# Optimization experiments

Hardware: AMD Instinct MI355X
Metric: run time of the kernel (lower is better)

Reference implementation:

```python
import jax, jax.numpy as jnp
import numpy as np

N = 100000   # nodes
E = 1000000  # edges
G = 2000     # graphs
ND = 64      # node_dim (== hidden_dim so per-layer params stack)
ED = 16      # edge_dim
HD = 64      # hidden_dim
L = 4        # num_layers


def setup_inputs() -> dict:
    key = jax.random.key(0)
    ks = jax.random.split(key, 16)
    s = 0.1  # param init scale
    return {
        "x": jax.random.normal(ks[0], (N, ND), jnp.float32),
        "edge_index": jax.random.randint(ks[1], (2, E), 0, N, jnp.int32),
        "edge_attr": jax.random.normal(ks[2], (E, ED), jnp.float32),
        "batch": jnp.sort(jax.random.randint(ks[3], (N,), 0, G, jnp.int32)),
        "t_cond": jax.random.uniform(ks[4], (G,), jnp.float32),
        # per-layer GINEConv params (stacked over L layers)
        "lin_e": jax.random.normal(ks[5], (L, ED, ND), jnp.float32) * s,  # edge_attr -> in_dim
        "W1": jax.random.normal(ks[6], (L, ND, HD), jnp.float32) * s,
        "b1": jnp.zeros((L, HD), jnp.float32),
        "W2": jax.random.normal(ks[7], (L, HD, HD), jnp.float32) * s,
        "b2": jnp.zeros((L, HD), jnp.float32),
        "eps": jnp.zeros((L,), jnp.float32),  # train_eps=True, init 0
        # head: Linear(HD+1 -> HD), ReLU, Linear(HD -> 1)
        "head_W1": jax.random.normal(ks[8], (HD + 1, HD), jnp.float32) * s,
        "head_b1": jnp.zeros((HD,), jnp.float32),
        "head_W2": jax.random.normal(ks[9], (HD, 1), jnp.float32) * s,
        "head_b2": jnp.zeros((1,), jnp.float32),
    }


def reference(x, edge_index, edge_attr, batch, t_cond,
              lin_e, W1, b1, W2, b2, eps,
              head_W1, head_b1, head_W2, head_b2):
    src = edge_index[0]  # x_j (message source)
    dst = edge_index[1]  # x_i (aggregation target)
    for l in range(L):
        # GINEConv: m_ij = ReLU(x_j + Lin(edge_attr)); aggr = sum_j m_ij
        e = edge_attr @ lin_e[l]                      # [E, ND]
        m = jax.nn.relu(x[src] + e)                   # gather + fuse
        aggr = jax.ops.segment_sum(m, dst, num_segments=N)  # scatter-add [N, ND]
        h = (1.0 + eps[l]) * x + aggr
        x = jax.nn.relu(h @ W1[l] + b1[l]) @ W2[l] + b2[l]  # nn_seq MLP
        x = jax.nn.relu(x)  # outer ReLU (dropout off at inference)
    # global mean pool over graphs
    sums = jax.ops.segment_sum(x, batch, num_segments=G)          # [G, HD]
    cnts = jax.ops.segment_sum(jnp.ones((N, 1), x.dtype), batch, num_segments=G)
    pooled = sums / jnp.maximum(cnts, 1.0)
    h = jnp.concatenate([pooled, t_cond[:, None].astype(x.dtype)], axis=-1)  # [G, HD+1]
    out = jax.nn.relu(h @ head_W1 + head_b1) @ head_W2 + head_b2             # [G, 1]
    return out
```

## Files before the change

kernel.cpp:

```cpp
#include <hip/hip_runtime.h>

#define NDIM 64
#define EDIM 16
#define SCAN_BS 256
#define SCAN_TILE 2048

typedef __attribute__((ext_vector_type(8))) short short8;
typedef __attribute__((ext_vector_type(4))) float f32x4;
typedef __attribute__((ext_vector_type(4))) float f4;

#define AS4 __attribute__((address_space(4)))
__device__ inline const AS4 int* cs_i(const int* p) {
    return (const AS4 int*)(unsigned long long)p;
}
__device__ inline const AS4 f4* cs_f4(const float* p) {
    return (const AS4 f4*)(unsigned long long)p;
}

__device__ inline unsigned short f2bf_rne(float f) {
    unsigned int u = __float_as_uint(f);
    unsigned int r = u + 0x7FFFu + ((u >> 16) & 1u);
    return (unsigned short)(r >> 16);
}
__device__ inline float bf2f(unsigned short h) {
    return __uint_as_float(((unsigned int)h) << 16);
}
__device__ inline void cvt8(const float4 v0, const float4 v1, short8& hi, short8& lo) {
    float v[8] = {v0.x, v0.y, v0.z, v0.w, v1.x, v1.y, v1.z, v1.w};
#pragma unroll
    for (int j = 0; j < 8; ++j) {
        unsigned short h = f2bf_rne(v[j]);
        hi[j] = (short)h;
        lo[j] = (short)f2bf_rne(v[j] - bf2f(h));
    }
}


__global__ __launch_bounds__(256) void hist_kernel(const int* __restrict__ edge_index,
                                                   int* __restrict__ deg, int E) {
    int e = blockIdx.x * blockDim.x + threadIdx.x;
    if (e < E) atomicAdd(&deg[edge_index[E + e]], 1);
}

__global__ __launch_bounds__(SCAN_BS) void scan_tile_kernel(const int* __restrict__ deg,
                                                            int* __restrict__ excl,
                                                            int* __restrict__ tsum, int n) {
    __shared__ int sdata[SCAN_BS];
    int base = blockIdx.x * SCAN_TILE + threadIdx.x * 8;
    int v[8]; int s = 0;
#pragma unroll
    for (int j = 0; j < 8; ++j) { int idx = base + j; int val = (idx < n) ? deg[idx] : 0; v[j] = val; s += val; }
    sdata[threadIdx.x] = s;
    __syncthreads();
    for (int off = 1; off < SCAN_BS; off <<= 1) {
        int t = (threadIdx.x >= (unsigned)off) ? sdata[threadIdx.x - off] : 0;
        __syncthreads();
        sdata[threadIdx.x] += t;
        __syncthreads();
    }
    int incl = sdata[threadIdx.x];
    if (threadIdx.x == SCAN_BS - 1) tsum[blockIdx.x] = incl;
    int run = incl - s;
#pragma unroll
    for (int j = 0; j < 8; ++j) { int idx = base + j; if (idx < n) excl[idx] = run; run += v[j]; }
}

__global__ void scan_sums_kernel(int* tsum, int ntiles) {
    if (threadIdx.x == 0 && blockIdx.x == 0) {
        int run = 0;
        for (int i = 0; i < ntiles; ++i) { int t = tsum[i]; tsum[i] = run; run += t; }
    }
}

__global__ __launch_bounds__(256) void scan_add_kernel(int* __restrict__ rowptr,
                                                       const int* __restrict__ tsum,
                                                       int* __restrict__ fillc, int n, int E) {
    int i = blockIdx.x * blockDim.x + threadIdx.x;
    if (i < n) {
        int v = rowptr[i] + tsum[i / SCAN_TILE];
        rowptr[i] = v;
        fillc[i] = v;
    }
    if (i == 0) rowptr[n] = E;
}

__global__ __launch_bounds__(256) void fill_kernel(const int* __restrict__ edge_index,
                                                   int* __restrict__ fillc,
                                                   int* __restrict__ srcs,
                                                   int* __restrict__ eids, int E) {
    int e = blockIdx.x * blockDim.x + threadIdx.x;
    if (e < E) {
        int d = edge_index[E + e];
        int pos = atomicAdd(&fillc[d], 1);
        srcs[pos] = edge_index[e];
        eids[pos] = e;
    }
}

__global__ __launch_bounds__(256) void permute_kernel(const int* __restrict__ eids,
                                                      const float4* __restrict__ ea,
                                                      float4* __restrict__ gea, int E) {
    int p = blockIdx.x * blockDim.x + threadIdx.x;
    if (p < E) {
        int e = eids[p];
        float4 r0 = ea[(size_t)e*4+0], r1 = ea[(size_t)e*4+1],
               r2 = ea[(size_t)e*4+2], r3 = ea[(size_t)e*4+3];
        size_t q = (size_t)p * 4;
        gea[q+0] = r0; gea[q+1] = r1; gea[q+2] = r2; gea[q+3] = r3;
    }
}

#define EDGE_FMA16(m, A0, A1, A2, A3)                                   \
    m = fmaf(A0.x, le[ 0], m); m = fmaf(A0.y, le[ 1], m);               \
    m = fmaf(A0.z, le[ 2], m); m = fmaf(A0.w, le[ 3], m);               \
    m = fmaf(A1.x, le[ 4], m); m = fmaf(A1.y, le[ 5], m);               \
    m = fmaf(A1.z, le[ 6], m); m = fmaf(A1.w, le[ 7], m);               \
    m = fmaf(A2.x, le[ 8], m); m = fmaf(A2.y, le[ 9], m);               \
    m = fmaf(A2.z, le[10], m); m = fmaf(A2.w, le[11], m);               \
    m = fmaf(A3.x, le[12], m); m = fmaf(A3.y, le[13], m);               \
    m = fmaf(A3.z, le[14], m); m = fmaf(A3.w, le[15], m);


__global__ __launch_bounds__(256) void aggr_kernel(
    const float* __restrict__ xin, float* __restrict__ hout,
    const int* __restrict__ rowptr, const int* __restrict__ srcs,
    const float* __restrict__ gea,
    const float* __restrict__ lin_e, const float* __restrict__ eps,
    int layer, int n_nodes)
{
    const int lane = threadIdx.x & 63;
    float le[16];
    const float* lep = lin_e + (size_t)layer * EDIM * NDIM;
#pragma unroll
    for (int j = 0; j < EDIM; ++j) le[j] = lep[j * NDIM + lane];
    const float eps1 = 1.0f + eps[layer];

    const AS4 int* rp = cs_i(rowptr);
    const AS4 int* sc = cs_i(srcs);

    int gw = __builtin_amdgcn_readfirstlane((int)((blockIdx.x * blockDim.x + threadIdx.x) >> 6));
    int nw = (gridDim.x * blockDim.x) >> 6;
    for (int node = gw; node < n_nodes; node += nw) {
        int p0 = rp[node], p1 = rp[node + 1];
        float aggr = 0.0f;
        int p = p0;
        for (; p + 4 <= p1; p += 4) {
            int s0 = sc[p], s1 = sc[p + 1], s2 = sc[p + 2], s3 = sc[p + 3];
            float xs0 = xin[(size_t)s0 * NDIM + lane];
            float xs1 = xin[(size_t)s1 * NDIM + lane];
            float xs2 = xin[(size_t)s2 * NDIM + lane];
            float xs3 = xin[(size_t)s3 * NDIM + lane];
            const AS4 f4* ea = cs_f4(gea + (size_t)p * EDIM);
            f4 a0 = ea[ 0], a1 = ea[ 1], a2 = ea[ 2], a3 = ea[ 3];
            f4 e0 = ea[ 4], e1 = ea[ 5], e2 = ea[ 6], e3 = ea[ 7];
            f4 c0 = ea[ 8], c1 = ea[ 9], c2 = ea[10], c3 = ea[11];
            f4 d0 = ea[12], d1 = ea[13], d2 = ea[14], d3 = ea[15];
            float m0 = xs0, m1 = xs1, m2 = xs2, m3 = xs3;
            EDGE_FMA16(m0, a0, a1, a2, a3)
            EDGE_FMA16(m1, e0, e1, e2, e3)
            EDGE_FMA16(m2, c0, c1, c2, c3)
            EDGE_FMA16(m3, d0, d1, d2, d3)
            aggr += fmaxf(m0, 0.0f) + fmaxf(m1, 0.0f) + fmaxf(m2, 0.0f) + fmaxf(m3, 0.0f);
        }
        for (; p < p1; ++p) {
            int s0 = sc[p];
            float xs0 = xin[(size_t)s0 * NDIM + lane];
            const AS4 f4* ea = cs_f4(gea + (size_t)p * EDIM);
            f4 a0 = ea[0], a1 = ea[1], a2 = ea[2], a3 = ea[3];
            float m0 = xs0;
            EDGE_FMA16(m0, a0, a1, a2, a3)
            aggr += fmaxf(m0, 0.0f);
        }
        hout[(size_t)node * NDIM + lane] = fmaf(eps1, xin[(size_t)node * NDIM + lane], aggr);
    }
}


__global__ __launch_bounds__(256) void mlp_mfma_kernel(
    float* __restrict__ h,
    const float* __restrict__ W1, const float* __restrict__ b1,
    const float* __restrict__ W2, const float* __restrict__ b2,
    int layer, int n_nodes)
{
    __shared__ unsigned short sW1hi[4096], sW1lo[4096], sW2hi[4096], sW2lo[4096];
    __shared__ float sY[4][16 * 64];

    const float* w1 = W1 + (size_t)layer * 4096;
    const float* w2 = W2 + (size_t)layer * 4096;
    for (int idx = threadIdx.x; idx < 4096; idx += 256) {
        int k = idx >> 6, n = idx & 63;
        int c = k >> 5, q = (k >> 3) & 3, j = k & 7;
        int fidx = ((c * 4 + q) * 64 + n) * 8 + j;
        float a = w1[idx];
        unsigned short hi = f2bf_rne(a);
        sW1hi[fidx] = hi;
        sW1lo[fidx] = f2bf_rne(a - bf2f(hi));
        float b = w2[idx];
        hi = f2bf_rne(b);
        sW2hi[fidx] = hi;
        sW2lo[fidx] = f2bf_rne(b - bf2f(hi));
    }
    __syncthreads();

    const int lane = threadIdx.x & 63;
    const int wid = threadIdx.x >> 6;
    const int m = lane & 15, q = lane >> 4;
    float* Y = sY[wid];

    float b1v[4], b2v[4];
#pragma unroll
    for (int nt = 0; nt < 4; ++nt) {
        b1v[nt] = b1[layer * 64 + m + nt * 16];
        b2v[nt] = b2[layer * 64 + m + nt * 16];
    }

    int tiles = (n_nodes + 15) >> 4;
    int gw = blockIdx.x * 4 + wid;
    int nw = gridDim.x * 4;
    for (int t = gw; t < tiles; t += nw) {
        int r0 = t << 4;
        int rA = r0 + m; if (rA > n_nodes - 1) rA = n_nodes - 1;
        const float* hrow = h + (size_t)rA * 64;

        short8 Ahi[2], Alo[2];
#pragma unroll
        for (int c = 0; c < 2; ++c) {
            const float4* hp = (const float4*)(hrow + c * 32 + q * 8);
            float4 v0 = hp[0], v1 = hp[1];
            cvt8(v0, v1, Ahi[c], Alo[c]);
        }

#pragma unroll
        for (int nt = 0; nt < 4; ++nt) {
            int col = m + nt * 16;
            f32x4 acc = {0.f, 0.f, 0.f, 0.f};
#pragma unroll
            for (int c = 0; c < 2; ++c) {
                short8 bh = *(const short8*)&sW1hi[((c * 4 + q) * 64 + col) * 8];
                short8 bl = *(const short8*)&sW1lo[((c * 4 + q) * 64 + col) * 8];
                acc = __builtin_amdgcn_mfma_f32_16x16x32_bf16(Ahi[c], bh, acc, 0, 0, 0);
                acc = __builtin_amdgcn_mfma_f32_16x16x32_bf16(Alo[c], bh, acc, 0, 0, 0);
                acc = __builtin_amdgcn_mfma_f32_16x16x32_bf16(Ahi[c], bl, acc, 0, 0, 0);
            }
#pragma unroll
            for (int i = 0; i < 4; ++i) {
                int row = q * 4 + i;
                float y = fmaxf(acc[i] + b1v[nt], 0.0f);
                int gran = ((m >> 2) + 4 * nt) ^ row;
                Y[(row << 6) + (gran << 2) + (m & 3)] = y;
            }
        }
        __asm__ volatile("s_waitcnt lgkmcnt(0)" ::: "memory");

        short8 Yhi[2], Ylo[2];
#pragma unroll
        for (int c = 0; c < 2; ++c) {
            int g0 = c * 8 + q * 2;
            float4 v0 = *(const float4*)&Y[(m << 6) + ((g0 ^ m) << 2)];
            float4 v1 = *(const float4*)&Y[(m << 6) + (((g0 + 1) ^ m) << 2)];
            cvt8(v0, v1, Yhi[c], Ylo[c]);
        }

#pragma unroll
        for (int nt = 0; nt < 4; ++nt) {
            int col = m + nt * 16;
            f32x4 acc = {0.f, 0.f, 0.f, 0.f};
#pragma unroll
            for (int c = 0; c < 2; ++c) {
                short8 bh = *(const short8*)&sW2hi[((c * 4 + q) * 64 + col) * 8];
                short8 bl = *(const short8*)&sW2lo[((c * 4 + q) * 64 + col) * 8];
                acc = __builtin_amdgcn_mfma_f32_16x16x32_bf16(Yhi[c], bh, acc, 0, 0, 0);
                acc = __builtin_amdgcn_mfma_f32_16x16x32_bf16(Ylo[c], bh, acc, 0, 0, 0);
                acc = __builtin_amdgcn_mfma_f32_16x16x32_bf16(Yhi[c], bl, acc, 0, 0, 0);
            }
#pragma unroll
            for (int i = 0; i < 4; ++i) {
                int row = r0 + q * 4 + i;
                if (row < n_nodes)
                    h[(size_t)row * 64 + col] = fmaxf(acc[i] + b2v[nt], 0.0f);
            }
        }
    }
}

__global__ __launch_bounds__(256) void layer_kernel(
    const float* __restrict__ xin, float* __restrict__ xout,
    const int* __restrict__ rowptr, const int* __restrict__ srcs, const int* __restrict__ eids,
    const float* __restrict__ edge_attr,
    const float* __restrict__ lin_e, const float* __restrict__ W1, const float* __restrict__ b1,
    const float* __restrict__ W2, const float* __restrict__ b2, const float* __restrict__ eps,
    int layer, int n_nodes)
{
    __shared__ float s_W1[NDIM * NDIM];
    __shared__ float s_W2[NDIM * NDIM];
    const float* w1 = W1 + (size_t)layer * NDIM * NDIM;
    const float* w2 = W2 + (size_t)layer * NDIM * NDIM;
    for (int i = threadIdx.x; i < NDIM * NDIM; i += 256) { s_W1[i] = w1[i]; s_W2[i] = w2[i]; }
    const int lane = threadIdx.x & 63;
    float le[16];
    const float* lep = lin_e + (size_t)layer * EDIM * NDIM;
#pragma unroll
    for (int j = 0; j < EDIM; ++j) le[j] = lep[j * NDIM + lane];
    const float bb1 = b1[layer * NDIM + lane];
    const float bb2 = b2[layer * NDIM + lane];
    const float eps1 = 1.0f + eps[layer];
    __syncthreads();
    int gw = (blockIdx.x * blockDim.x + threadIdx.x) >> 6;
    int nw = (gridDim.x * blockDim.x) >> 6;
    for (int node = gw; node < n_nodes; node += nw) {
        int p0 = rowptr[node], p1 = rowptr[node + 1];
        float aggr = 0.0f;
        for (int p = p0; p < p1; ++p) {
            int s = srcs[p];
            int e = eids[p];
            float xs = xin[(size_t)s * NDIM + lane];
            const float4* ea = (const float4*)(edge_attr + (size_t)e * EDIM);
            float4 a0 = ea[0], a1 = ea[1], a2 = ea[2], a3 = ea[3];
            float m0 = xs;
            EDGE_FMA16(m0, a0, a1, a2, a3)
            aggr += fmaxf(m0, 0.0f);
        }
        float h = fmaf(eps1, xin[(size_t)node * NDIM + lane], aggr);
        float o1 = bb1;
#pragma unroll 8
        for (int k = 0; k < NDIM; ++k) o1 = fmaf(__shfl(h, k), s_W1[k * NDIM + lane], o1);
        o1 = fmaxf(o1, 0.0f);
        float o2 = bb2;
#pragma unroll 8
        for (int k = 0; k < NDIM; ++k) o2 = fmaf(__shfl(o1, k), s_W2[k * NDIM + lane], o2);
        xout[(size_t)node * NDIM + lane] = fmaxf(o2, 0.0f);
    }
}


__global__ __launch_bounds__(256) void starts_kernel(const int* __restrict__ batch,
                                                     int* __restrict__ starts, int N, int G) {
    int g = blockIdx.x * blockDim.x + threadIdx.x;
    if (g <= G) {
        int lo = 0, hi = N;
        while (lo < hi) { int mid = (lo + hi) >> 1; if (batch[mid] < g) lo = mid + 1; else hi = mid; }
        starts[g] = lo;
    }
}

__global__ __launch_bounds__(256) void poolhead_kernel(const float* __restrict__ x,
                                                       const int* __restrict__ starts,
                                                       const float* __restrict__ t_cond,
                                                       const float* __restrict__ hW1,
                                                       const float* __restrict__ hb1,
                                                       const float* __restrict__ hW2,
                                                       const float* __restrict__ hb2,
                                                       float* __restrict__ out, int G) {
    __shared__ float sW1[(NDIM + 1) * NDIM];
    __shared__ float sb1[NDIM];
    __shared__ float sW2[NDIM];
    for (int i = threadIdx.x; i < (NDIM + 1) * NDIM; i += 256) sW1[i] = hW1[i];
    if (threadIdx.x < NDIM) { sb1[threadIdx.x] = hb1[threadIdx.x]; sW2[threadIdx.x] = hW2[threadIdx.x]; }
    __syncthreads();
    const int lane = threadIdx.x & 63;
    int gw = (blockIdx.x * blockDim.x + threadIdx.x) >> 6;
    int nw = (gridDim.x * blockDim.x) >> 6;
    for (int g = gw; g < G; g += nw) {
        int a = starts[g], b = starts[g + 1];
        float s0 = 0.0f, s1 = 0.0f, s2 = 0.0f, s3 = 0.0f;
        int n = a;
        for (; n + 4 <= b; n += 4) {
            s0 += x[(size_t)n * NDIM + lane];
            s1 += x[(size_t)(n + 1) * NDIM + lane];
            s2 += x[(size_t)(n + 2) * NDIM + lane];
            s3 += x[(size_t)(n + 3) * NDIM + lane];
        }
        for (; n < b; ++n) s0 += x[(size_t)n * NDIM + lane];
        float c = fmaxf((float)(b - a), 1.0f);
        float p = ((s0 + s1) + (s2 + s3)) / c;
        float t = t_cond[g];
        float o1 = fmaf(t, sW1[NDIM * NDIM + lane], sb1[lane]);
#pragma unroll 8
        for (int k = 0; k < NDIM; ++k) o1 = fmaf(__shfl(p, k), sW1[k * NDIM + lane], o1);
        o1 = fmaxf(o1, 0.0f);
        float v = o1 * sW2[lane];
        for (int off = 32; off > 0; off >>= 1) v += __shfl_down(v, off);
        if (lane == 0) out[g] = v + hb2[0];
    }
}


extern "C" void kernel_launch(void* const* d_in, const int* in_sizes, int n_in,
                              void* d_out, int out_size, void* d_ws, size_t ws_size,
                              hipStream_t stream) {
    const float* x_in      = (const float*)d_in[0];
    const int*   edge_index= (const int*)  d_in[1];
    const float* edge_attr = (const float*)d_in[2];
    const int*   batch     = (const int*)  d_in[3];
    const float* t_cond    = (const float*)d_in[4];
    const float* lin_e     = (const float*)d_in[5];
    const float* W1        = (const float*)d_in[6];
    const float* b1        = (const float*)d_in[7];
    const float* W2        = (const float*)d_in[8];
    const float* b2        = (const float*)d_in[9];
    const float* eps       = (const float*)d_in[10];
    const float* hW1       = (const float*)d_in[11];
    const float* hb1       = (const float*)d_in[12];
    const float* hW2       = (const float*)d_in[13];
    const float* hb2       = (const float*)d_in[14];
    float* out = (float*)d_out;

    const int N = in_sizes[3];
    const int E = in_sizes[1] / 2;
    const int G = in_sizes[4];
    const int L = in_sizes[10];
    const int ntiles = (N + SCAN_TILE - 1) / SCAN_TILE;

    char* p = (char*)d_ws;
    auto alloc = [&](size_t bytes) { char* r = p; p += (bytes + 255) & ~(size_t)255; return r; };
    int*   rowptr = (int*)  alloc((size_t)(N + 1) * 4);
    int*   fillc  = (int*)  alloc((size_t)N * 4);
    int*   srcs   = (int*)  alloc((size_t)E * 4);
    int*   tsum   = (int*)  alloc((size_t)ntiles * 4);
    int*   starts = (int*)  alloc((size_t)(G + 1) * 4);
    float* bufA   = (float*)alloc((size_t)N * NDIM * 4);
    float* bufB   = (float*)alloc((size_t)N * NDIM * 4);
    size_t base_used = (size_t)(p - (char*)d_ws);
    float* gea    = (float*)alloc((size_t)E * EDIM * 4);
    bool use_gea = (base_used + (size_t)E * EDIM * 4) <= ws_size
                   && (size_t)E * 4 <= (size_t)N * NDIM * 4;
    int* eids = use_gea ? (int*)bufA : (int*)((char*)d_ws + base_used);

    hipMemsetAsync(fillc, 0, (size_t)N * 4, stream);
    hist_kernel<<<(E + 255) / 256, 256, 0, stream>>>(edge_index, fillc, E);
    scan_tile_kernel<<<ntiles, SCAN_BS, 0, stream>>>(fillc, rowptr, tsum, N);
    scan_sums_kernel<<<1, 64, 0, stream>>>(tsum, ntiles);
    scan_add_kernel<<<(N + 255) / 256, 256, 0, stream>>>(rowptr, tsum, fillc, N, E);
    fill_kernel<<<(E + 255) / 256, 256, 0, stream>>>(edge_index, fillc, srcs, eids, E);
    if (use_gea) {
        permute_kernel<<<(E + 255) / 256, 256, 0, stream>>>(eids, (const float4*)edge_attr,
                                                            (float4*)gea, E);
    }
    starts_kernel<<<(G + 256) / 256, 256, 0, stream>>>(batch, starts, N, G);

    const float* cur = x_in;
    float* work = bufA;
    for (int l = 0; l < L; ++l) {
        if (use_gea) {
            aggr_kernel<<<2048, 256, 0, stream>>>(cur, work, rowptr, srcs, gea, lin_e, eps, l, N);
            mlp_mfma_kernel<<<1024, 256, 0, stream>>>(work, W1, b1, W2, b2, l, N);
            cur = work;
            work = (work == bufA) ? bufB : bufA;
        } else {
            layer_kernel<<<1024, 256, 0, stream>>>(cur, work, rowptr, srcs, eids,
                                                   edge_attr, lin_e, W1, b1, W2, b2, eps, l, N);
            cur = work;
            work = (work == bufA) ? bufB : bufA;
        }
    }

    poolhead_kernel<<<512, 256, 0, stream>>>(cur, starts, t_cond, hW1, hb1, hW2, hb2, out, G);
}
```

Before: 689.0 us.

## Replace per-node CSR aggregation with edge-balanced flat aggregation using boundary atomics

```diff
diff --git a/kernel.cpp b/kernel.cpp
--- a/kernel.cpp
+++ b/kernel.cpp
@@ -86,27 +86,44 @@
 
 __global__ __launch_bounds__(256) void fill_kernel(const int* __restrict__ edge_index,
                                                    int* __restrict__ fillc,
-                                                   int* __restrict__ srcs,
                                                    int* __restrict__ eids, int E) {
     int e = blockIdx.x * blockDim.x + threadIdx.x;
     if (e < E) {
         int d = edge_index[E + e];
         int pos = atomicAdd(&fillc[d], 1);
-        srcs[pos] = edge_index[e];
         eids[pos] = e;
     }
 }
 
 __global__ __launch_bounds__(256) void permute_kernel(const int* __restrict__ eids,
+                                                      const int* __restrict__ edge_index,
                                                       const float4* __restrict__ ea,
-                                                      float4* __restrict__ gea, int E) {
+                                                      float4* __restrict__ gea,
+                                                      int* __restrict__ srcs,
+                                                      int* __restrict__ gdst, int E) {
     int p = blockIdx.x * blockDim.x + threadIdx.x;
     if (p < E) {
         int e = eids[p];
+        srcs[p] = edge_index[e];
+        gdst[p] = edge_index[E + e];
         float4 r0 = ea[(size_t)e*4+0], r1 = ea[(size_t)e*4+1],
                r2 = ea[(size_t)e*4+2], r3 = ea[(size_t)e*4+3];
         size_t q = (size_t)p * 4;
         gea[q+0] = r0; gea[q+1] = r1; gea[q+2] = r2; gea[q+3] = r3;
+    }
+}
+
+__global__ __launch_bounds__(256) void init_h_kernel(const float4* __restrict__ x,
+                                                     float4* __restrict__ h,
+                                                     const float* __restrict__ eps,
+                                                     int layer, int n4) {
+    float e1 = 1.0f + eps[layer];
+    int i = blockIdx.x * blockDim.x + threadIdx.x;
+    int stride = gridDim.x * blockDim.x;
+    for (; i < n4; i += stride) {
+        float4 v = x[i];
+        v.x *= e1; v.y *= e1; v.z *= e1; v.w *= e1;
+        h[i] = v;
     }
 }
 
@@ -121,58 +138,74 @@
     m = fmaf(A3.z, le[14], m); m = fmaf(A3.w, le[15], m);
 
 
-__global__ __launch_bounds__(256) void aggr_kernel(
-    const float* __restrict__ xin, float* __restrict__ hout,
-    const int* __restrict__ rowptr, const int* __restrict__ srcs,
+__global__ __launch_bounds__(256) void aggr_flat_kernel(
+    const float* __restrict__ xin, float* __restrict__ hacc,
+    const int* __restrict__ srcs, const int* __restrict__ gdst,
     const float* __restrict__ gea,
-    const float* __restrict__ lin_e, const float* __restrict__ eps,
-    int layer, int n_nodes)
+    const float* __restrict__ lin_e, int layer, int E)
 {
     const int lane = threadIdx.x & 63;
     float le[16];
     const float* lep = lin_e + (size_t)layer * EDIM * NDIM;
 #pragma unroll
     for (int j = 0; j < EDIM; ++j) le[j] = lep[j * NDIM + lane];
-    const float eps1 = 1.0f + eps[layer];
-
-    const AS4 int* rp = cs_i(rowptr);
+
     const AS4 int* sc = cs_i(srcs);
-
-    int gw = __builtin_amdgcn_readfirstlane((int)((blockIdx.x * blockDim.x + threadIdx.x) >> 6));
-    int nw = (gridDim.x * blockDim.x) >> 6;
-    for (int node = gw; node < n_nodes; node += nw) {
-        int p0 = rp[node], p1 = rp[node + 1];
-        float aggr = 0.0f;
-        int p = p0;
-        for (; p + 4 <= p1; p += 4) {
-            int s0 = sc[p], s1 = sc[p + 1], s2 = sc[p + 2], s3 = sc[p + 3];
-            float xs0 = xin[(size_t)s0 * NDIM + lane];
-            float xs1 = xin[(size_t)s1 * NDIM + lane];
-            float xs2 = xin[(size_t)s2 * NDIM + lane];
-            float xs3 = xin[(size_t)s3 * NDIM + lane];
-            const AS4 f4* ea = cs_f4(gea + (size_t)p * EDIM);
-            f4 a0 = ea[ 0], a1 = ea[ 1], a2 = ea[ 2], a3 = ea[ 3];
-            f4 e0 = ea[ 4], e1 = ea[ 5], e2 = ea[ 6], e3 = ea[ 7];
-            f4 c0 = ea[ 8], c1 = ea[ 9], c2 = ea[10], c3 = ea[11];
-            f4 d0 = ea[12], d1 = ea[13], d2 = ea[14], d3 = ea[15];
-            float m0 = xs0, m1 = xs1, m2 = xs2, m3 = xs3;
-            EDGE_FMA16(m0, a0, a1, a2, a3)
-            EDGE_FMA16(m1, e0, e1, e2, e3)
-            EDGE_FMA16(m2, c0, c1, c2, c3)
-            EDGE_FMA16(m3, d0, d1, d2, d3)
-            aggr += fmaxf(m0, 0.0f) + fmaxf(m1, 0.0f) + fmaxf(m2, 0.0f) + fmaxf(m3, 0.0f);
-        }
-        for (; p < p1; ++p) {
-            int s0 = sc[p];
-            float xs0 = xin[(size_t)s0 * NDIM + lane];
-            const AS4 f4* ea = cs_f4(gea + (size_t)p * EDIM);
-            f4 a0 = ea[0], a1 = ea[1], a2 = ea[2], a3 = ea[3];
-            float m0 = xs0;
-            EDGE_FMA16(m0, a0, a1, a2, a3)
-            aggr += fmaxf(m0, 0.0f);
-        }
-        hout[(size_t)node * NDIM + lane] = fmaf(eps1, xin[(size_t)node * NDIM + lane], aggr);
-    }
+    const AS4 int* dc = cs_i(gdst);
+
+    int w = (blockIdx.x * blockDim.x + threadIdx.x) >> 6;
+    int W = (gridDim.x * blockDim.x) >> 6;
+    int S = (E + W - 1) / W;
+    int p    = __builtin_amdgcn_readfirstlane(w * S);
+    int pend = __builtin_amdgcn_readfirstlane(min(E, p + S));
+    if (p >= pend) return;
+
+    float aggr = 0.0f;
+    int dprev = dc[p];
+    for (; p + 4 <= pend; p += 4) {
+        int s0 = sc[p], s1 = sc[p+1], s2 = sc[p+2], s3 = sc[p+3];
+        int d0 = dc[p], d1 = dc[p+1], d2 = dc[p+2], d3 = dc[p+3];
+        float xs0 = xin[(size_t)s0 * NDIM + lane];
+        float xs1 = xin[(size_t)s1 * NDIM + lane];
+        float xs2 = xin[(size_t)s2 * NDIM + lane];
+        float xs3 = xin[(size_t)s3 * NDIM + lane];
+        const AS4 f4* ea = cs_f4(gea + (size_t)p * EDIM);
+        f4 a0 = ea[ 0], a1 = ea[ 1], a2 = ea[ 2], a3 = ea[ 3];
+        f4 e0 = ea[ 4], e1 = ea[ 5], e2 = ea[ 6], e3 = ea[ 7];
+        f4 c0 = ea[ 8], c1 = ea[ 9], c2 = ea[10], c3 = ea[11];
+        f4 g0 = ea[12], g1 = ea[13], g2 = ea[14], g3 = ea[15];
+        float m0 = xs0, m1 = xs1, m2 = xs2, m3 = xs3;
+        EDGE_FMA16(m0, a0, a1, a2, a3)
+        EDGE_FMA16(m1, e0, e1, e2, e3)
+        EDGE_FMA16(m2, c0, c1, c2, c3)
+        EDGE_FMA16(m3, g0, g1, g2, g3)
+        m0 = fmaxf(m0, 0.0f); m1 = fmaxf(m1, 0.0f);
+        m2 = fmaxf(m2, 0.0f); m3 = fmaxf(m3, 0.0f);
+        if (d3 == dprev) {
+            aggr += (m0 + m1) + (m2 + m3);
+        } else {
+            if (d0 != dprev) { atomicAdd(&hacc[(size_t)dprev * NDIM + lane], aggr); aggr = 0.0f; dprev = d0; }
+            aggr += m0;
+            if (d1 != dprev) { atomicAdd(&hacc[(size_t)dprev * NDIM + lane], aggr); aggr = 0.0f; dprev = d1; }
+            aggr += m1;
+            if (d2 != dprev) { atomicAdd(&hacc[(size_t)dprev * NDIM + lane], aggr); aggr = 0.0f; dprev = d2; }
+            aggr += m2;
+            if (d3 != dprev) { atomicAdd(&hacc[(size_t)dprev * NDIM + lane], aggr); aggr = 0.0f; dprev = d3; }
+            aggr += m3;
+        }
+    }
+    for (; p < pend; ++p) {
+        int s0 = sc[p];
+        int d0 = dc[p];
+        float xs0 = xin[(size_t)s0 * NDIM + lane];
+        const AS4 f4* ea = cs_f4(gea + (size_t)p * EDIM);
+        f4 a0 = ea[0], a1 = ea[1], a2 = ea[2], a3 = ea[3];
+        float m0 = xs0;
+        EDGE_FMA16(m0, a0, a1, a2, a3)
+        if (d0 != dprev) { atomicAdd(&hacc[(size_t)dprev * NDIM + lane], aggr); aggr = 0.0f; dprev = d0; }
+        aggr += fmaxf(m0, 0.0f);
+    }
+    atomicAdd(&hacc[(size_t)dprev * NDIM + lane], aggr);
 }
 
 
@@ -285,11 +318,12 @@
 
 __global__ __launch_bounds__(256) void layer_kernel(
     const float* __restrict__ xin, float* __restrict__ xout,
-    const int* __restrict__ rowptr, const int* __restrict__ srcs, const int* __restrict__ eids,
+    const int* __restrict__ rowptr, const int* __restrict__ eids,
+    const int* __restrict__ edge_index,
     const float* __restrict__ edge_attr,
     const float* __restrict__ lin_e, const float* __restrict__ W1, const float* __restrict__ b1,
     const float* __restrict__ W2, const float* __restrict__ b2, const float* __restrict__ eps,
-    int layer, int n_nodes)
+    int layer, int n_nodes, int E)
 {
     __shared__ float s_W1[NDIM * NDIM];
     __shared__ float s_W2[NDIM * NDIM];
@@ -311,8 +345,8 @@
         int p0 = rowptr[node], p1 = rowptr[node + 1];
         float aggr = 0.0f;
         for (int p = p0; p < p1; ++p) {
-            int s = srcs[p];
             int e = eids[p];
+            int s = edge_index[e];
             float xs = xin[(size_t)s * NDIM + lane];
             const float4* ea = (const float4*)(edge_attr + (size_t)e * EDIM);
             float4 a0 = ea[0], a1 = ea[1], a2 = ea[2], a3 = ea[3];
@@ -416,6 +450,7 @@
     int*   rowptr = (int*)  alloc((size_t)(N + 1) * 4);
     int*   fillc  = (int*)  alloc((size_t)N * 4);
     int*   srcs   = (int*)  alloc((size_t)E * 4);
+    int*   gdst   = (int*)  alloc((size_t)E * 4);
     int*   tsum   = (int*)  alloc((size_t)ntiles * 4);
     int*   starts = (int*)  alloc((size_t)(G + 1) * 4);
     float* bufA   = (float*)alloc((size_t)N * NDIM * 4);
@@ -424,33 +459,36 @@
     float* gea    = (float*)alloc((size_t)E * EDIM * 4);
     bool use_gea = (base_used + (size_t)E * EDIM * 4) <= ws_size
                    && (size_t)E * 4 <= (size_t)N * NDIM * 4;
-    int* eids = use_gea ? (int*)bufA : (int*)((char*)d_ws + base_used);
+    int* eids = (int*)bufA;
 
     hipMemsetAsync(fillc, 0, (size_t)N * 4, stream);
     hist_kernel<<<(E + 255) / 256, 256, 0, stream>>>(edge_index, fillc, E);
     scan_tile_kernel<<<ntiles, SCAN_BS, 0, stream>>>(fillc, rowptr, tsum, N);
     scan_sums_kernel<<<1, 64, 0, stream>>>(tsum, ntiles);
     scan_add_kernel<<<(N + 255) / 256, 256, 0, stream>>>(rowptr, tsum, fillc, N, E);
-    fill_kernel<<<(E + 255) / 256, 256, 0, stream>>>(edge_index, fillc, srcs, eids, E);
+    fill_kernel<<<(E + 255) / 256, 256, 0, stream>>>(edge_index, fillc, eids, E);
     if (use_gea) {
-        permute_kernel<<<(E + 255) / 256, 256, 0, stream>>>(eids, (const float4*)edge_attr,
-                                                            (float4*)gea, E);
+        permute_kernel<<<(E + 255) / 256, 256, 0, stream>>>(eids, edge_index, (const float4*)edge_attr,
+                                                            (float4*)gea, srcs, gdst, E);
     }
     starts_kernel<<<(G + 256) / 256, 256, 0, stream>>>(batch, starts, N, G);
 
+    const int n4 = N * NDIM / 4;
     const float* cur = x_in;
     float* work = bufA;
     for (int l = 0; l < L; ++l) {
         if (use_gea) {
-            aggr_kernel<<<2048, 256, 0, stream>>>(cur, work, rowptr, srcs, gea, lin_e, eps, l, N);
+            init_h_kernel<<<2048, 256, 0, stream>>>((const float4*)cur, (float4*)work, eps, l, n4);
+            aggr_flat_kernel<<<2048, 256, 0, stream>>>(cur, work, srcs, gdst, gea, lin_e, l, E);
             mlp_mfma_kernel<<<1024, 256, 0, stream>>>(work, W1, b1, W2, b2, l, N);
             cur = work;
             work = (work == bufA) ? bufB : bufA;
         } else {
-            layer_kernel<<<1024, 256, 0, stream>>>(cur, work, rowptr, srcs, eids,
-                                                   edge_attr, lin_e, W1, b1, W2, b2, eps, l, N);
-            cur = work;
-            work = (work == bufA) ? bufB : bufA;
+            float* tgt = (l == 0) ? bufB : work;
+            layer_kernel<<<1024, 256, 0, stream>>>(cur, tgt, rowptr, eids, edge_index,
+                                                   edge_attr, lin_e, W1, b1, W2, b2, eps, l, N, E);
+            cur = tgt;
+            work = (tgt == bufA) ? bufB : bufA;
         }
     }
 
```

Result: no change. 699.0 us (+1.5%).
